# Optimization experiments

Hardware: AMD Instinct MI355X
Metric: run time of the kernel (lower is better)

## Reference

```python
import jax, jax.numpy as jnp
import numpy as np

NUM_PINS = 10_000_000
NUM_NETS = 3_000_000


def setup_inputs() -> dict:
    key = jax.random.key(0)
    k1, k2 = jax.random.split(key)
    pos = jax.random.normal(k1, (2 * NUM_PINS,), dtype=jnp.float32) * 1000.0
    pin2net_map = jax.random.randint(k2, (NUM_PINS,), 0, NUM_NETS, dtype=jnp.int32)
    net_mask = jnp.ones((NUM_NETS,), dtype=bool)
    return {"pos": pos, "pin2net_map": pin2net_map, "net_mask": net_mask}


def reference(pos, pin2net_map, net_mask):
    # pos: [2*num_pins]; first half = x coords, second half = y coords
    num_pins = pos.shape[0] // 2
    num_nets = net_mask.shape[0]
    x = pos[:num_pins]
    y = pos[num_pins:]

    # per-net bounding box via segment min/max (the atomic scatter reduction)
    xmax = jax.ops.segment_max(x, pin2net_map, num_segments=num_nets)
    xmin = jax.ops.segment_min(x, pin2net_map, num_segments=num_nets)
    ymax = jax.ops.segment_max(y, pin2net_map, num_segments=num_nets)
    ymin = jax.ops.segment_min(y, pin2net_map, num_segments=num_nets)

    # nets with no pins would yield (-inf) - (+inf); mask them out
    counts = jax.ops.segment_sum(jnp.ones_like(x), pin2net_map, num_segments=num_nets)
    valid = net_mask & (counts > 0)

    hpwl_per_net = (xmax - xmin) + (ymax - ymin)
    total = jnp.sum(jnp.where(valid, hpwl_per_net, jnp.float32(0.0)))
    return total.reshape(1)
```

## Files before the change

### kernel.cpp

```cpp
#include <hip/hip_runtime.h>


#define BK_SHIFT 13
#define BK_NETS  8192
#define NBK_MAX  368
#define SUB      4992
#define NSUB     4
#define CHUNK    (SUB * NSUB)
#define TPB      1024
#define RTPB     1024
#define CAP      29440

typedef float v4f __attribute__((ext_vector_type(4)));
typedef int   v4i __attribute__((ext_vector_type(4)));

__device__ __forceinline__ unsigned enc(float f) {
    unsigned u = __float_as_uint(f);
    return u ^ ((unsigned)((int)u >> 31) | 0x80000000u);
}
__device__ __forceinline__ float dec(unsigned u) {
    unsigned b = (u & 0x80000000u) ? (u ^ 0x80000000u) : ~u;
    return __uint_as_float(b);
}
__device__ __forceinline__ uint2 pack_rec(float x, float y, int net) {
    unsigned ex = enc(x), ey = enc(y);
    unsigned n = (unsigned)net;
    uint2 r;
    r.x = (ex & ~2047u) | (n >> 11);
    r.y = (ey & ~2047u) | (n & 2047u);
    return r;
}

__global__ __launch_bounds__(TPB) void scatter_kernel(
        const float* __restrict__ pos, const int* __restrict__ p2n,
        unsigned* __restrict__ gcur,
        uint2* __restrict__ recs,
        float* __restrict__ out,
        int P, int NBK) {
    __shared__ uint2    stage[SUB];
    __shared__ unsigned hist4[NSUB * NBK_MAX];
    __shared__ unsigned slab[NBK_MAX];
    __shared__ unsigned fc[NBK_MAX];
    __shared__ unsigned scur[NBK_MAX];
    __shared__ unsigned wbase[NBK_MAX];
    __shared__ unsigned wsum[TPB / 64];

    const int b = blockIdx.x;
    if (b == 0 && threadIdx.x == 0) *out = 0.0f;
    const int pstart = b * CHUNK;
    const int pcount = min(P - pstart, CHUNK);

    for (int k = threadIdx.x; k < NSUB * NBK_MAX; k += TPB) hist4[k] = 0;
    __syncthreads();

    int nv = pcount >> 2;
    for (int g = threadIdx.x; g < nv; g += TPB) {
        v4i n4 = *(const v4i*)(p2n + pstart + (g << 2));
        unsigned* h = &hist4[(g / (SUB >> 2)) * NBK_MAX];
        atomicAdd(&h[n4.x >> BK_SHIFT], 1u);
        atomicAdd(&h[n4.y >> BK_SHIFT], 1u);
        atomicAdd(&h[n4.z >> BK_SHIFT], 1u);
        atomicAdd(&h[n4.w >> BK_SHIFT], 1u);
    }
    __syncthreads();

    for (int k = threadIdx.x; k < NBK; k += TPB) {
        unsigned c = 0;
        #pragma unroll
        for (int s = 0; s < NSUB; ++s) c += hist4[s * NBK_MAX + k];
        slab[k] = c ? atomicAdd(&gcur[k], c) : 0u;
        fc[k] = 0;
    }
    __syncthreads();

    for (int s = 0; s < NSUB; ++s) {
        int sbase = pstart + s * SUB;
        int scount = min(pcount - s * SUB, SUB);
        if (scount <= 0) break;
        int snv = scount >> 2;
        const unsigned* hs = &hist4[s * NBK_MAX];

        {
            int t = threadIdx.x;
            unsigned v = (t < NBK) ? hs[t] : 0u;
            unsigned x = v;
            #pragma unroll
            for (int off = 1; off < 64; off <<= 1) {
                unsigned y = __shfl_up(x, (unsigned)off);
                if ((t & 63) >= off) x += y;
            }
            if ((t & 63) == 63) wsum[t >> 6] = x;
            __syncthreads();
            if (t < 64) {
                unsigned w = (t < (TPB / 64)) ? wsum[t] : 0u;
                unsigned xx = w;
                #pragma unroll
                for (int off = 1; off < (TPB / 64); off <<= 1) {
                    unsigned y = __shfl_up(xx, (unsigned)off);
                    if (t >= off) xx += y;
                }
                if (t < (TPB / 64)) wsum[t] = xx - w;
            }
            __syncthreads();
            if (t < NBK) {
                unsigned e = x - v + wsum[t >> 6];
                scur[t] = e;
                wbase[t] = slab[t] + fc[t] - e;
                fc[t] += v;
            }
            __syncthreads();
        }

        for (int g = threadIdx.x; g < snv; g += TPB) {
            int p = sbase + (g << 2);
            v4i n4 = *(const v4i*)(p2n + p);
            v4f xs = __builtin_nontemporal_load((const v4f*)(pos + p));
            v4f ys = __builtin_nontemporal_load((const v4f*)(pos + P + p));
            unsigned s0 = atomicAdd(&scur[n4.x >> BK_SHIFT], 1u);
            stage[s0] = pack_rec(xs.x, ys.x, n4.x);
            unsigned s1 = atomicAdd(&scur[n4.y >> BK_SHIFT], 1u);
            stage[s1] = pack_rec(xs.y, ys.y, n4.y);
            unsigned s2 = atomicAdd(&scur[n4.z >> BK_SHIFT], 1u);
            stage[s2] = pack_rec(xs.z, ys.z, n4.z);
            unsigned s3 = atomicAdd(&scur[n4.w >> BK_SHIFT], 1u);
            stage[s3] = pack_rec(xs.w, ys.w, n4.w);
        }
        __syncthreads();

        for (int i = threadIdx.x; i < scount; i += TPB) {
            uint2 r = stage[i];
            int bk = (int)((r.x & 2047u) >> 2);
            unsigned off = wbase[bk] + (unsigned)i;
            if (off < CAP)
                recs[(size_t)bk * CAP + off] = r;
        }
        __syncthreads();
    }
}

__global__ __launch_bounds__(RTPB) void reduce_kernel(
        const uint2* __restrict__ recs,
        const unsigned* __restrict__ gcur,
        const int* __restrict__ mask,
        float* __restrict__ out, int num_nets) {
    int k = blockIdx.x;
    __shared__ unsigned tile[4 * BK_NETS];
    for (int i = threadIdx.x; i < 4 * BK_NETS; i += RTPB) tile[i] = 0;
    __syncthreads();

    unsigned cnt = min(gcur[k], (unsigned)CAP);
    const uint2* base = recs + (size_t)k * CAP;
    const uint4* b4 = (const uint4*)base;
    unsigned nv = cnt >> 1;
    for (unsigned i = threadIdx.x; i < nv; i += RTPB) {
        uint4 q = b4[i];
        unsigned nl0 = ((q.x & 3u) << 11) | (q.y & 2047u);
        unsigned ex0 = q.x & ~2047u, ey0 = q.y & ~2047u;
        atomicMax(&tile[nl0], ex0);
        atomicMax(&tile[BK_NETS + nl0], (~ex0) & ~2047u);
        atomicMax(&tile[2 * BK_NETS + nl0], ey0);
        atomicMax(&tile[3 * BK_NETS + nl0], (~ey0) & ~2047u);
        unsigned nl1 = ((q.z & 3u) << 11) | (q.w & 2047u);
        unsigned ex1 = q.z & ~2047u, ey1 = q.w & ~2047u;
        atomicMax(&tile[nl1], ex1);
        atomicMax(&tile[BK_NETS + nl1], (~ex1) & ~2047u);
        atomicMax(&tile[2 * BK_NETS + nl1], ey1);
        atomicMax(&tile[3 * BK_NETS + nl1], (~ey1) & ~2047u);
    }
    if ((cnt & 1u) && threadIdx.x == 0) {
        uint2 r = base[cnt - 1];
        unsigned nl = ((r.x & 3u) << 11) | (r.y & 2047u);
        unsigned ex = r.x & ~2047u, ey = r.y & ~2047u;
        atomicMax(&tile[nl], ex);
        atomicMax(&tile[BK_NETS + nl], (~ex) & ~2047u);
        atomicMax(&tile[2 * BK_NETS + nl], ey);
        atomicMax(&tile[3 * BK_NETS + nl], (~ey) & ~2047u);
    }
    __syncthreads();

    int gbase = k << BK_SHIFT;
    int nthis = min(BK_NETS, num_nets - gbase);
    float h = 0.0f;
    for (int n = threadIdx.x; n < nthis; n += RTPB) {
        unsigned a = tile[n];
        if (a != 0u && mask[gbase + n] != 0) {
            float xmax = dec(a);
            float xmin = dec(~tile[BK_NETS + n]);
            float ymax = dec(tile[2 * BK_NETS + n]);
            float ymin = dec(~tile[3 * BK_NETS + n]);
            h += (xmax - xmin) + (ymax - ymin);
        }
    }

    #pragma unroll
    for (int off = 32; off > 0; off >>= 1)
        h += __shfl_down(h, off);
    __syncthreads();
    float* ws = (float*)tile;
    if ((threadIdx.x & 63) == 0) ws[threadIdx.x >> 6] = h;
    __syncthreads();
    if (threadIdx.x == 0) {
        float t = 0.0f;
        #pragma unroll
        for (int w = 0; w < RTPB / 64; ++w) t += ws[w];
        atomicAdd(out, t);
    }
}

__device__ __forceinline__ void upd(unsigned* __restrict__ nets,
                                    float x, float y, int net) {
    unsigned ex = enc(x), ey = enc(y);
    unsigned* base = nets + ((size_t)net << 2);
    atomicMax(base + 0, ex);
    atomicMax(base + 1, ~ex);
    atomicMax(base + 2, ey);
    atomicMax(base + 3, ~ey);
}

__global__ void fb_pin_kernel(const float* __restrict__ pos,
                              const int* __restrict__ p2n,
                              unsigned* __restrict__ nets, int num_pins) {
    int i = blockIdx.x * blockDim.x + threadIdx.x;
    if (i >= num_pins) return;
    upd(nets, pos[i], pos[i + num_pins], p2n[i]);
}

__global__ void fb_net_kernel(const uint4* __restrict__ nets,
                              const int* __restrict__ mask,
                              float* __restrict__ out, int num_nets) {
    int i = blockIdx.x * blockDim.x + threadIdx.x;
    float h = 0.0f;
    if (i < num_nets) {
        uint4 v = nets[i];
        if (v.x != 0u && mask[i] != 0)
            h = (dec(v.x) - dec(~v.y)) + (dec(v.z) - dec(~v.w));
    }
    #pragma unroll
    for (int off = 32; off > 0; off >>= 1)
        h += __shfl_down(h, off);
    __shared__ float s[4];
    int wid = threadIdx.x >> 6;
    if ((threadIdx.x & 63) == 0) s[wid] = h;
    __syncthreads();
    if (threadIdx.x == 0)
        atomicAdd(out, s[0] + s[1] + s[2] + s[3]);
}

extern "C" void kernel_launch(void* const* d_in, const int* in_sizes, int n_in,
                              void* d_out, int out_size, void* d_ws, size_t ws_size,
                              hipStream_t stream) {
    const float* pos = (const float*)d_in[0];
    const int* p2n = (const int*)d_in[1];
    const int* mask = (const int*)d_in[2];
    const int P = in_sizes[0] / 2;
    const int N = in_sizes[2];

    const int NBK = (N + BK_NETS - 1) >> BK_SHIFT;
    const int NB = (P + CHUNK - 1) / CHUNK;

    size_t recs_bytes = (size_t)NBK * CAP * sizeof(uint2);
    size_t need = recs_bytes + (size_t)NBK * sizeof(unsigned) + 256;

    size_t mean_load = (NBK > 0) ? (size_t)P / (size_t)NBK : 0;
    size_t slack = 8 * (size_t)(__builtin_sqrt((double)(mean_load + 1))) + 512;
    bool cap_ok = (NBK > 0) && (mean_load + slack <= CAP);

    if (NBK > 0 && NBK <= NBK_MAX && (P & 3) == 0 && ws_size >= need && cap_ok) {
        uint2* recs = (uint2*)d_ws;
        unsigned* gcur = (unsigned*)((char*)d_ws + recs_bytes);
        hipMemsetAsync(gcur, 0, (size_t)NBK * sizeof(unsigned), stream);

        scatter_kernel<<<NB, TPB, 0, stream>>>(pos, p2n, gcur, recs,
                                               (float*)d_out, P, NBK);
        reduce_kernel<<<NBK, RTPB, 0, stream>>>(recs, gcur, mask, (float*)d_out, N);
    } else {
        unsigned* nets = (unsigned*)d_ws;
        hipMemsetAsync(d_out, 0, sizeof(float), stream);
        hipMemsetAsync(d_ws, 0, (size_t)N * 4 * sizeof(unsigned), stream);
        fb_pin_kernel<<<(P + 255) / 256, 256, 0, stream>>>(pos, p2n, nets, P);
        fb_net_kernel<<<(N + 255) / 256, 256, 0, stream>>>((const uint4*)nets, mask,
                                                           (float*)d_out, N);
    }
}
```

Baseline: 215.8 us.

## Reuse histogram atomic return values as stage ranks, removing second atomic pass

The histogram pass now keeps the value returned by each LDS atomicAdd as the element's rank within its bucket, packed as 16-bit pairs in registers. The scatter pass then places each record at a precomputed bucket start plus that rank, with no second round of shared-memory atomics. To fit one vec4 group per thread per sub-chunk, sub-chunk size changes from 4992 to 4096 and the count from 4 to 5, with the sub-chunk loop fully unrolled. This adds register pressure and the chunk now holds 20480 pins instead of 19968, which changes the grid size and per-bucket load.

New measurement: 222.8 us. 1.03x slower.

```diff
diff --git a/kernel.cpp b/kernel.cpp
--- a/kernel.cpp
+++ b/kernel.cpp
@@ -4,8 +4,8 @@
 #define BK_SHIFT 13
 #define BK_NETS  8192
 #define NBK_MAX  368
-#define SUB      4992
-#define NSUB     4
+#define SUB      4096
+#define NSUB     5
 #define CHUNK    (SUB * NSUB)
 #define TPB      1024
 #define RTPB     1024
@@ -41,7 +41,7 @@
     __shared__ unsigned hist4[NSUB * NBK_MAX];
     __shared__ unsigned slab[NBK_MAX];
     __shared__ unsigned fc[NBK_MAX];
-    __shared__ unsigned scur[NBK_MAX];
+    __shared__ unsigned sstart[NBK_MAX];
     __shared__ unsigned wbase[NBK_MAX];
     __shared__ unsigned wsum[TPB / 64];
 
@@ -54,13 +54,20 @@
     __syncthreads();
 
     int nv = pcount >> 2;
-    for (int g = threadIdx.x; g < nv; g += TPB) {
-        v4i n4 = *(const v4i*)(p2n + pstart + (g << 2));
-        unsigned* h = &hist4[(g / (SUB >> 2)) * NBK_MAX];
-        atomicAdd(&h[n4.x >> BK_SHIFT], 1u);
-        atomicAdd(&h[n4.y >> BK_SHIFT], 1u);
-        atomicAdd(&h[n4.z >> BK_SHIFT], 1u);
-        atomicAdd(&h[n4.w >> BK_SHIFT], 1u);
+    unsigned rk01[NSUB], rk23[NSUB];
+    #pragma unroll
+    for (int s = 0; s < NSUB; ++s) {
+        int g = (s << 10) + threadIdx.x;
+        if (g < nv) {
+            v4i n4 = *(const v4i*)(p2n + pstart + (g << 2));
+            unsigned* h = &hist4[s * NBK_MAX];
+            unsigned a0 = atomicAdd(&h[n4.x >> BK_SHIFT], 1u);
+            unsigned a1 = atomicAdd(&h[n4.y >> BK_SHIFT], 1u);
+            unsigned a2 = atomicAdd(&h[n4.z >> BK_SHIFT], 1u);
+            unsigned a3 = atomicAdd(&h[n4.w >> BK_SHIFT], 1u);
+            rk01[s] = a0 | (a1 << 16);
+            rk23[s] = a2 | (a3 << 16);
+        }
     }
     __syncthreads();
 
@@ -73,68 +80,71 @@
     }
     __syncthreads();
 
+    #pragma unroll
     for (int s = 0; s < NSUB; ++s) {
-        int sbase = pstart + s * SUB;
         int scount = min(pcount - s * SUB, SUB);
-        if (scount <= 0) break;
-        int snv = scount >> 2;
-        const unsigned* hs = &hist4[s * NBK_MAX];
-
-        {
-            int t = threadIdx.x;
-            unsigned v = (t < NBK) ? hs[t] : 0u;
-            unsigned x = v;
-            #pragma unroll
-            for (int off = 1; off < 64; off <<= 1) {
-                unsigned y = __shfl_up(x, (unsigned)off);
-                if ((t & 63) >= off) x += y;
+        if (scount > 0) {
+            const unsigned* hs = &hist4[s * NBK_MAX];
+
+            {
+                int t = threadIdx.x;
+                unsigned v = (t < NBK) ? hs[t] : 0u;
+                unsigned x = v;
+                #pragma unroll
+                for (int off = 1; off < 64; off <<= 1) {
+                    unsigned y = __shfl_up(x, (unsigned)off);
+                    if ((t & 63) >= off) x += y;
+                }
+                if ((t & 63) == 63) wsum[t >> 6] = x;
+                __syncthreads();
+                if (t < 64) {
+                    unsigned w = (t < (TPB / 64)) ? wsum[t] : 0u;
+                    unsigned xx = w;
+                    #pragma unroll
+                    for (int off = 1; off < (TPB / 64); off <<= 1) {
+                        unsigned y = __shfl_up(xx, (unsigned)off);
+                        if (t >= off) xx += y;
+                    }
+                    if (t < (TPB / 64)) wsum[t] = xx - w;
+                }
+                __syncthreads();
+                if (t < NBK) {
+                    unsigned e = x - v + wsum[t >> 6];
+                    sstart[t] = e;
+                    wbase[t] = slab[t] + fc[t] - e;
+                    fc[t] += v;
+                }
+                __syncthreads();
             }
-            if ((t & 63) == 63) wsum[t >> 6] = x;
-            __syncthreads();
-            if (t < 64) {
-                unsigned w = (t < (TPB / 64)) ? wsum[t] : 0u;
-                unsigned xx = w;
-                #pragma unroll
-                for (int off = 1; off < (TPB / 64); off <<= 1) {
-                    unsigned y = __shfl_up(xx, (unsigned)off);
-                    if (t >= off) xx += y;
-                }
-                if (t < (TPB / 64)) wsum[t] = xx - w;
+
+            {
+                int g = (s << 10) + threadIdx.x;
+                if (g < nv) {
+                    int p = pstart + (g << 2);
+                    v4i n4 = *(const v4i*)(p2n + p);
+                    v4f xs = __builtin_nontemporal_load((const v4f*)(pos + p));
+                    v4f ys = __builtin_nontemporal_load((const v4f*)(pos + P + p));
+                    stage[sstart[n4.x >> BK_SHIFT] + (rk01[s] & 0xffffu)] =
+                        pack_rec(xs.x, ys.x, n4.x);
+                    stage[sstart[n4.y >> BK_SHIFT] + (rk01[s] >> 16)] =
+                        pack_rec(xs.y, ys.y, n4.y);
+                    stage[sstart[n4.z >> BK_SHIFT] + (rk23[s] & 0xffffu)] =
+                        pack_rec(xs.z, ys.z, n4.z);
+                    stage[sstart[n4.w >> BK_SHIFT] + (rk23[s] >> 16)] =
+                        pack_rec(xs.w, ys.w, n4.w);
+                }
             }
             __syncthreads();
-            if (t < NBK) {
-                unsigned e = x - v + wsum[t >> 6];
-                scur[t] = e;
-                wbase[t] = slab[t] + fc[t] - e;
-                fc[t] += v;
+
+            for (int i = threadIdx.x; i < scount; i += TPB) {
+                uint2 r = stage[i];
+                int bk = (int)((r.x & 2047u) >> 2);
+                unsigned off = wbase[bk] + (unsigned)i;
+                if (off < CAP)
+                    recs[(size_t)bk * CAP + off] = r;
             }
             __syncthreads();
         }
-
-        for (int g = threadIdx.x; g < snv; g += TPB) {
-            int p = sbase + (g << 2);
-            v4i n4 = *(const v4i*)(p2n + p);
-            v4f xs = __builtin_nontemporal_load((const v4f*)(pos + p));
-            v4f ys = __builtin_nontemporal_load((const v4f*)(pos + P + p));
-            unsigned s0 = atomicAdd(&scur[n4.x >> BK_SHIFT], 1u);
-            stage[s0] = pack_rec(xs.x, ys.x, n4.x);
-            unsigned s1 = atomicAdd(&scur[n4.y >> BK_SHIFT], 1u);
-            stage[s1] = pack_rec(xs.y, ys.y, n4.y);
-            unsigned s2 = atomicAdd(&scur[n4.z >> BK_SHIFT], 1u);
-            stage[s2] = pack_rec(xs.z, ys.z, n4.z);
-            unsigned s3 = atomicAdd(&scur[n4.w >> BK_SHIFT], 1u);
-            stage[s3] = pack_rec(xs.w, ys.w, n4.w);
-        }
-        __syncthreads();
-
-        for (int i = threadIdx.x; i < scount; i += TPB) {
-            uint2 r = stage[i];
-            int bk = (int)((r.x & 2047u) >> 2);
-            unsigned off = wbase[bk] + (unsigned)i;
-            if (off < CAP)
-                recs[(size_t)bk * CAP + off] = r;
-        }
-        __syncthreads();
     }
 }
 
```

## Pad per-block bucket slabs to 16 records and enlarge scatter chunks

Applied to the files above, without the earlier changes.

Each scatter block now reserves bucket space in multiples of 16 records and fills the padding with zero records. Bucket slabs use a power-of-two stride, and sub-chunks grow from 4992 to 6144 pins, so there are fewer blocks. The aim is aligned, full-line global writes per slab, and a reduce loop that drops its odd-tail path by skipping zero records. The costs are the extra padding writes, the extra zero checks in the reduce, more workspace use, and a tighter capacity margin.

Result: slower. 227.6 us (+5.4%).

```diff
diff --git a/kernel.cpp b/kernel.cpp
--- a/kernel.cpp
+++ b/kernel.cpp
@@ -4,12 +4,13 @@
 #define BK_SHIFT 13
 #define BK_NETS  8192
 #define NBK_MAX  368
-#define SUB      4992
+#define SUB      6144
 #define NSUB     4
 #define CHUNK    (SUB * NSUB)
 #define TPB      1024
 #define RTPB     1024
-#define CAP      29440
+#define CAP      32768
+#define CAP_SHIFT 15
 
 typedef float v4f __attribute__((ext_vector_type(4)));
 typedef int   v4i __attribute__((ext_vector_type(4)));
@@ -68,7 +69,8 @@
         unsigned c = 0;
         #pragma unroll
         for (int s = 0; s < NSUB; ++s) c += hist4[s * NBK_MAX + k];
-        slab[k] = c ? atomicAdd(&gcur[k], c) : 0u;
+        unsigned c16 = (c + 15u) & ~15u;
+        slab[k] = c16 ? atomicAdd(&gcur[k], c16) : 0u;
         fc[k] = 0;
     }
     __syncthreads();
@@ -132,9 +134,25 @@
             int bk = (int)((r.x & 2047u) >> 2);
             unsigned off = wbase[bk] + (unsigned)i;
             if (off < CAP)
-                recs[(size_t)bk * CAP + off] = r;
+                recs[((size_t)bk << CAP_SHIFT) + off] = r;
         }
         __syncthreads();
+    }
+
+    {
+        int wid = threadIdx.x >> 6, lane = threadIdx.x & 63, nw = TPB >> 6;
+        for (int k = wid; k < NBK; k += nw) {
+            unsigned c = fc[k];
+            unsigned c16 = (c + 15u) & ~15u;
+            unsigned j = c + (unsigned)lane;
+            if (j < c16) {
+                unsigned off = slab[k] + j;
+                if (off < CAP) {
+                    uint2 z; z.x = 0u; z.y = 0u;
+                    recs[((size_t)k << CAP_SHIFT) + off] = z;
+                }
+            }
+        }
     }
 }
 
@@ -149,32 +167,27 @@
     __syncthreads();
 
     unsigned cnt = min(gcur[k], (unsigned)CAP);
-    const uint2* base = recs + (size_t)k * CAP;
+    const uint2* base = recs + ((size_t)k << CAP_SHIFT);
     const uint4* b4 = (const uint4*)base;
     unsigned nv = cnt >> 1;
     for (unsigned i = threadIdx.x; i < nv; i += RTPB) {
         uint4 q = b4[i];
-        unsigned nl0 = ((q.x & 3u) << 11) | (q.y & 2047u);
-        unsigned ex0 = q.x & ~2047u, ey0 = q.y & ~2047u;
-        atomicMax(&tile[nl0], ex0);
-        atomicMax(&tile[BK_NETS + nl0], (~ex0) & ~2047u);
-        atomicMax(&tile[2 * BK_NETS + nl0], ey0);
-        atomicMax(&tile[3 * BK_NETS + nl0], (~ey0) & ~2047u);
-        unsigned nl1 = ((q.z & 3u) << 11) | (q.w & 2047u);
-        unsigned ex1 = q.z & ~2047u, ey1 = q.w & ~2047u;
-        atomicMax(&tile[nl1], ex1);
-        atomicMax(&tile[BK_NETS + nl1], (~ex1) & ~2047u);
-        atomicMax(&tile[2 * BK_NETS + nl1], ey1);
-        atomicMax(&tile[3 * BK_NETS + nl1], (~ey1) & ~2047u);
-    }
-    if ((cnt & 1u) && threadIdx.x == 0) {
-        uint2 r = base[cnt - 1];
-        unsigned nl = ((r.x & 3u) << 11) | (r.y & 2047u);
-        unsigned ex = r.x & ~2047u, ey = r.y & ~2047u;
-        atomicMax(&tile[nl], ex);
-        atomicMax(&tile[BK_NETS + nl], (~ex) & ~2047u);
-        atomicMax(&tile[2 * BK_NETS + nl], ey);
-        atomicMax(&tile[3 * BK_NETS + nl], (~ey) & ~2047u);
+        if (q.x) {
+            unsigned nl0 = ((q.x & 3u) << 11) | (q.y & 2047u);
+            unsigned ex0 = q.x & ~2047u, ey0 = q.y & ~2047u;
+            atomicMax(&tile[nl0], ex0);
+            atomicMax(&tile[BK_NETS + nl0], (~ex0) & ~2047u);
+            atomicMax(&tile[2 * BK_NETS + nl0], ey0);
+            atomicMax(&tile[3 * BK_NETS + nl0], (~ey0) & ~2047u);
+        }
+        if (q.z) {
+            unsigned nl1 = ((q.z & 3u) << 11) | (q.w & 2047u);
+            unsigned ex1 = q.z & ~2047u, ey1 = q.w & ~2047u;
+            atomicMax(&tile[nl1], ex1);
+            atomicMax(&tile[BK_NETS + nl1], (~ex1) & ~2047u);
+            atomicMax(&tile[2 * BK_NETS + nl1], ey1);
+            atomicMax(&tile[3 * BK_NETS + nl1], (~ey1) & ~2047u);
+        }
     }
     __syncthreads();
 
@@ -262,8 +275,9 @@
     size_t need = recs_bytes + (size_t)NBK * sizeof(unsigned) + 256;
 
     size_t mean_load = (NBK > 0) ? (size_t)P / (size_t)NBK : 0;
+    size_t pad_mean = (size_t)NB * 8;
     size_t slack = 8 * (size_t)(__builtin_sqrt((double)(mean_load + 1))) + 512;
-    bool cap_ok = (NBK > 0) && (mean_load + slack <= CAP);
+    bool cap_ok = (NBK > 0) && (mean_load + pad_mean + slack <= CAP);
 
     if (NBK > 0 && NBK <= NBK_MAX && (P & 3) == 0 && ws_size >= need && cap_ok) {
         uint2* recs = (uint2*)d_ws;
```
